# Kernel optimization log

Hardware: AMD Instinct MI355X
Metric: run time of the kernel (lower is better)

## Reference

```python
import jax, jax.numpy as jnp
import numpy as np

# Sampled-block sizes (fanouts [25, 10], batch of 1024 seeds)
N_SRC1, N_DST1, N_E1 = 292864, 11264, 281600
N_DST2, N_E2 = 1024, 10240
IN, H, C = 256, 256, 47


def setup_inputs() -> dict:
    key = jax.random.key(0)
    ks = jax.random.split(key, 9)
    s_in = 1.0 / np.sqrt(IN)
    s_h = 1.0 / np.sqrt(H)
    x = jax.random.normal(ks[0], (N_SRC1, IN), jnp.float32)
    src1 = jax.random.randint(ks[1], (N_E1,), 0, N_SRC1)
    dst1 = jnp.sort(jax.random.randint(ks[2], (N_E1,), 0, N_DST1))
    src2 = jax.random.randint(ks[3], (N_E2,), 0, N_DST1)
    dst2 = jnp.sort(jax.random.randint(ks[4], (N_E2,), 0, N_DST2))
    return dict(
        x=x, src1=src1, dst1=dst1, src2=src2, dst2=dst2,
        W_self1=jax.random.normal(ks[5], (IN, H), jnp.float32) * s_in,
        W_neigh1=jax.random.normal(ks[6], (IN, H), jnp.float32) * s_in,
        b1=jnp.zeros((H,), jnp.float32),
        W_self2=jax.random.normal(ks[7], (H, C), jnp.float32) * s_h,
        W_neigh2=jax.random.normal(ks[8], (H, C), jnp.float32) * s_h,
        b2=jnp.zeros((C,), jnp.float32),
    )


def _sage_mean(h_src, src, dst, n_dst, W_self, W_neigh, b):
    # DGL SAGEConv(mean): out = fc_self(h_dst) + fc_neigh(mean_{neighbors} h_src) + b
    gathered = h_src[src]                                   # [E, F] gather
    agg = jax.ops.segment_sum(gathered, dst, num_segments=n_dst)
    deg = jax.ops.segment_sum(jnp.ones((src.shape[0],), h_src.dtype), dst,
                              num_segments=n_dst)
    h_neigh = agg / jnp.maximum(deg, 1.0)[:, None]          # mean aggregation
    h_dst = h_src[:n_dst]                                   # dst nodes are prefix of src
    return h_dst @ W_self + h_neigh @ W_neigh + b


def reference(x, src1, dst1, src2, dst2,
              W_self1, W_neigh1, b1, W_self2, W_neigh2, b2):
    h = _sage_mean(x, src1, dst1, N_DST1, W_self1, W_neigh1, b1)
    h = jax.nn.relu(h)  # dropout is identity in eval mode
    out = _sage_mean(h, src2, dst2, N_DST2, W_self2, W_neigh2, b2)
    return out
```

## Files before the change

### kernel.cpp

```cpp
#include <hip/hip_runtime.h>

#define NSRC1 292864
#define NDST1 11264
#define NE1   281600
#define NDST2 1024
#define NE2   10240

typedef __bf16 bf16x8 __attribute__((ext_vector_type(8)));
typedef float  f32x4  __attribute__((ext_vector_type(4)));

__device__ __forceinline__ unsigned short f2bf(float f) {
    union { float f; unsigned u; } v; v.f = f;
    unsigned r = v.u + 0x7FFF + ((v.u >> 16) & 1);
    return (unsigned short)(r >> 16);
}

__device__ __forceinline__ void acc4(float4& a, const float4& v) {
    a.x += v.x; a.y += v.y; a.z += v.z; a.w += v.w;
}

__global__ __launch_bounds__(256) void prep_kernel(
    const int* __restrict__ dst1, const int* __restrict__ dst2,
    const float* __restrict__ Ws, const float* __restrict__ Wn,
    int* __restrict__ rp1, int* __restrict__ rp2,
    unsigned short* __restrict__ Wt)
{
    __shared__ float t[64][65];
    if (blockIdx.x < 1140) {
        const int tid = blockIdx.x * 256 + threadIdx.x;
        if (tid < NE1) {
            const int d  = dst1[tid];
            const int dp = (tid == 0) ? -1 : dst1[tid - 1];
            for (int j = dp + 1; j <= d; ++j) rp1[j] = tid;
            if (tid == NE1 - 1) for (int j = d + 1; j <= NDST1; ++j) rp1[j] = NE1;
        } else {
            const int e  = tid - NE1;
            const int d  = dst2[e];
            const int dp = (e == 0) ? -1 : dst2[e - 1];
            for (int j = dp + 1; j <= d; ++j) rp2[j] = e;
            if (e == NE2 - 1) for (int j = d + 1; j <= NDST2; ++j) rp2[j] = NE2;
        }
        return;
    }
    const int tileid = blockIdx.x - 1140;
    const int kb = (tileid & 7) * 64, nb = (tileid >> 3) * 64;
    const float* __restrict__ W = (kb < 256) ? Ws : Wn;
    const int kofs = (kb < 256) ? kb : kb - 256;
    const int c  = threadIdx.x & 63;
    const int r0 = threadIdx.x >> 6;
    #pragma unroll
    for (int i = 0; i < 16; ++i) {
        const int r = r0 + i * 4;
        t[r][c] = W[(size_t)(kofs + r) * 256 + nb + c];
    }
    __syncthreads();
    #pragma unroll
    for (int i = 0; i < 16; ++i) {
        const int r = r0 + i * 4;
        Wt[(size_t)(nb + r) * 512 + kb + c] = f2bf(t[c][r]);
    }
}

__global__ __launch_bounds__(256) void agg1_fused_kernel(
    const float* __restrict__ x,
    const int*   __restrict__ src_idx,
    const int*   __restrict__ rowptr,
    unsigned short* __restrict__ Abf)
{
    const int lane = threadIdx.x & 63;
    const int w    = threadIdx.x >> 6;
    const int d    = blockIdx.x * 4 + w;

    const int start = rowptr[d];
    const int end   = rowptr[d + 1];

    const float4* __restrict__ xcol = (const float4*)x + lane;

    const float4 xv = xcol[(size_t)d * 64];

    float4 a0 = make_float4(0.f,0.f,0.f,0.f);
    float4 a1 = a0, a2 = a0, a3 = a0, a4 = a0, a5 = a0, a6 = a0, a7 = a0;

    for (int base = start; base < end; base += 64) {
        const int nb = (end - base < 64) ? (end - base) : 64;
        int my = (lane < nb) ? src_idx[base + lane] : 0;
        int j = 0;
        for (; j + 8 <= nb; j += 8) {
            const int s0 = __builtin_amdgcn_readlane(my, j + 0);
            const int s1 = __builtin_amdgcn_readlane(my, j + 1);
            const int s2 = __builtin_amdgcn_readlane(my, j + 2);
            const int s3 = __builtin_amdgcn_readlane(my, j + 3);
            const int s4 = __builtin_amdgcn_readlane(my, j + 4);
            const int s5 = __builtin_amdgcn_readlane(my, j + 5);
            const int s6 = __builtin_amdgcn_readlane(my, j + 6);
            const int s7 = __builtin_amdgcn_readlane(my, j + 7);
            const float4 v0 = xcol[(size_t)s0 * 64];
            const float4 v1 = xcol[(size_t)s1 * 64];
            const float4 v2 = xcol[(size_t)s2 * 64];
            const float4 v3 = xcol[(size_t)s3 * 64];
            const float4 v4 = xcol[(size_t)s4 * 64];
            const float4 v5 = xcol[(size_t)s5 * 64];
            const float4 v6 = xcol[(size_t)s6 * 64];
            const float4 v7 = xcol[(size_t)s7 * 64];
            acc4(a0, v0); acc4(a1, v1); acc4(a2, v2); acc4(a3, v3);
            acc4(a4, v4); acc4(a5, v5); acc4(a6, v6); acc4(a7, v7);
        }
        if (j + 4 <= nb) {
            const int s0 = __builtin_amdgcn_readlane(my, j + 0);
            const int s1 = __builtin_amdgcn_readlane(my, j + 1);
            const int s2 = __builtin_amdgcn_readlane(my, j + 2);
            const int s3 = __builtin_amdgcn_readlane(my, j + 3);
            const float4 v0 = xcol[(size_t)s0 * 64];
            const float4 v1 = xcol[(size_t)s1 * 64];
            const float4 v2 = xcol[(size_t)s2 * 64];
            const float4 v3 = xcol[(size_t)s3 * 64];
            acc4(a0, v0); acc4(a1, v1); acc4(a2, v2); acc4(a3, v3);
            j += 4;
        }
        for (; j < nb; ++j) {
            const int s = __builtin_amdgcn_readlane(my, j);
            acc4(a0, xcol[(size_t)s * 64]);
        }
    }
    acc4(a0, a1); acc4(a2, a3); acc4(a4, a5); acc4(a6, a7);
    acc4(a0, a2); acc4(a4, a6); acc4(a0, a4);

    const int deg = end - start;
    const float inv = 1.0f / (deg > 0 ? (float)deg : 1.0f);

    ushort4 nbv;
    nbv.x = f2bf(a0.x * inv); nbv.y = f2bf(a0.y * inv);
    nbv.z = f2bf(a0.z * inv); nbv.w = f2bf(a0.w * inv);
    *(ushort4*)(Abf + (size_t)d * 512 + 256 + lane * 4) = nbv;

    ushort4 sf;
    sf.x = f2bf(xv.x); sf.y = f2bf(xv.y); sf.z = f2bf(xv.z); sf.w = f2bf(xv.w);
    *(ushort4*)(Abf + (size_t)d * 512 + lane * 4) = sf;
}

#define LDT 40

__global__ __launch_bounds__(256) void gemm1_mfma_kernel(
    const unsigned short* __restrict__ Abf,
    const unsigned short* __restrict__ Wt,
    const float* __restrict__ bias,
    float* __restrict__ h)
{
    __shared__ unsigned short As[64][LDT];
    __shared__ unsigned short Bs[64][LDT];

    const int tid  = threadIdx.x;
    const int lane = tid & 63;
    const int w    = tid >> 6;
    const int wm   = (w & 1) * 32;
    const int wn   = (w >> 1) * 32;
    const int mblk = blockIdx.x * 64;
    const int nblk = blockIdx.y * 64;

    const int r16 = lane & 15;
    const int k0  = (lane >> 4) * 8;

    f32x4 acc[2][2] = {};

    for (int kt = 0; kt < 512; kt += 32) {
        {
            const int r  = tid >> 2;
            const int kk = (tid & 3) * 8;
            *(uint4*)&As[r][kk] =
                *(const uint4*)(Abf + (size_t)(mblk + r) * 512 + kt + kk);
            *(uint4*)&Bs[r][kk] =
                *(const uint4*)(Wt + (size_t)(nblk + r) * 512 + kt + kk);
        }
        __syncthreads();

        bf16x8 bfrag[2];
        #pragma unroll
        for (int ni = 0; ni < 2; ++ni)
            bfrag[ni] = *(const bf16x8*)&Bs[wn + ni * 16 + r16][k0];
        #pragma unroll
        for (int mi = 0; mi < 2; ++mi) {
            const bf16x8 afrag = *(const bf16x8*)&As[wm + mi * 16 + r16][k0];
            #pragma unroll
            for (int ni = 0; ni < 2; ++ni)
                acc[mi][ni] = __builtin_amdgcn_mfma_f32_16x16x32_bf16(
                    afrag, bfrag[ni], acc[mi][ni], 0, 0, 0);
        }
        __syncthreads();
    }

    #pragma unroll
    for (int mi = 0; mi < 2; ++mi) {
        #pragma unroll
        for (int ni = 0; ni < 2; ++ni) {
            const int col = nblk + wn + ni * 16 + r16;
            const float bb = bias[col];
            #pragma unroll
            for (int r = 0; r < 4; ++r) {
                const int row = mblk + wm + mi * 16 + (lane >> 4) * 4 + r;
                const float v = acc[mi][ni][r] + bb;
                h[(size_t)row * 256 + col] = v > 0.f ? v : 0.f;
            }
        }
    }
}

__global__ __launch_bounds__(256) void layer2_kernel(
    const float* __restrict__ h,
    const int*   __restrict__ src_idx,
    const int*   __restrict__ rowptr,
    const float* __restrict__ Ws,
    const float* __restrict__ Wn,
    const float* __restrict__ b,
    float* __restrict__ out)
{
    __shared__ float hn[4][260];
    __shared__ float hs[4][260];

    const int lane = threadIdx.x & 63;
    const int w    = threadIdx.x >> 6;
    const int m    = blockIdx.x * 4 + w;

    const int start = rowptr[m];
    const int end   = rowptr[m + 1];

    const float4* __restrict__ hcol = (const float4*)h + lane;

    const float4 sv = hcol[(size_t)m * 64];

    float4 a0 = make_float4(0.f,0.f,0.f,0.f);
    float4 a1 = a0, a2 = a0, a3 = a0;

    for (int base = start; base < end; base += 64) {
        const int nb = (end - base < 64) ? (end - base) : 64;
        int my = (lane < nb) ? src_idx[base + lane] : 0;
        int j = 0;
        for (; j + 4 <= nb; j += 4) {
            const int s0 = __builtin_amdgcn_readlane(my, j + 0);
            const int s1 = __builtin_amdgcn_readlane(my, j + 1);
            const int s2 = __builtin_amdgcn_readlane(my, j + 2);
            const int s3 = __builtin_amdgcn_readlane(my, j + 3);
            const float4 v0 = hcol[(size_t)s0 * 64];
            const float4 v1 = hcol[(size_t)s1 * 64];
            const float4 v2 = hcol[(size_t)s2 * 64];
            const float4 v3 = hcol[(size_t)s3 * 64];
            acc4(a0, v0); acc4(a1, v1); acc4(a2, v2); acc4(a3, v3);
        }
        for (; j < nb; ++j) {
            const int s = __builtin_amdgcn_readlane(my, j);
            acc4(a0, hcol[(size_t)s * 64]);
        }
    }
    acc4(a0, a1); acc4(a2, a3); acc4(a0, a2);

    const int deg = end - start;
    const float inv = 1.0f / (deg > 0 ? (float)deg : 1.0f);
    a0.x *= inv; a0.y *= inv; a0.z *= inv; a0.w *= inv;
    *(float4*)&hn[w][lane * 4] = a0;
    *(float4*)&hs[w][lane * 4] = sv;
    __syncthreads();

    if (lane < 47) {
        float acc = b[lane];
        #pragma unroll 4
        for (int k = 0; k < 256; ++k) {
            acc += hs[w][k] * Ws[k * 47 + lane] + hn[w][k] * Wn[k * 47 + lane];
        }
        out[(size_t)m * 47 + lane] = acc;
    }
}

extern "C" void kernel_launch(void* const* d_in, const int* in_sizes, int n_in,
                              void* d_out, int out_size, void* d_ws, size_t ws_size,
                              hipStream_t stream) {
    const float* x    = (const float*)d_in[0];
    const int*   src1 = (const int*)  d_in[1];
    const int*   dst1 = (const int*)  d_in[2];
    const int*   src2 = (const int*)  d_in[3];
    const int*   dst2 = (const int*)  d_in[4];
    const float* Ws1  = (const float*)d_in[5];
    const float* Wn1  = (const float*)d_in[6];
    const float* b1   = (const float*)d_in[7];
    const float* Ws2  = (const float*)d_in[8];
    const float* Wn2  = (const float*)d_in[9];
    const float* b2   = (const float*)d_in[10];
    float* out = (float*)d_out;

    char* ws = (char*)d_ws;
    const size_t sz_Abf = (size_t)NDST1 * 512 * sizeof(unsigned short);
    const size_t sz_h   = (size_t)NDST1 * 256 * sizeof(float);
    const size_t sz_Wt  = (size_t)256 * 512 * sizeof(unsigned short);
    const size_t sz_rp1 = (size_t)(NDST1 + 2) * sizeof(int);
    unsigned short* Abf = (unsigned short*)(ws);
    float*          h   = (float*)(ws + sz_Abf);
    unsigned short* Wt  = (unsigned short*)(ws + sz_Abf + sz_h);
    int*            rp1 = (int*)(ws + sz_Abf + sz_h + sz_Wt);
    int*            rp2 = (int*)(ws + sz_Abf + sz_h + sz_Wt + sz_rp1);

    prep_kernel<<<1172, 256, 0, stream>>>(dst1, dst2, Ws1, Wn1, rp1, rp2, Wt);
    agg1_fused_kernel<<<NDST1 / 4, 256, 0, stream>>>(x, src1, rp1, Abf);
    dim3 g1(NDST1 / 64, 256 / 64);
    gemm1_mfma_kernel<<<g1, 256, 0, stream>>>(Abf, Wt, b1, h);
    layer2_kernel<<<NDST2 / 4, 256, 0, stream>>>(h, src2, rp2, Ws2, Wn2, b2, out);
}
```

Baseline: 440.3 us.

## Fuse layer-1 neighbor aggregation into the MFMA GEMM via shared-memory A tile

Merges the gather/mean aggregation kernel and the layer-1 GEMM into one kernel. Each block aggregates 16 destination rows into an LDS A tile in bf16, then multiplies it by all 256 output columns using MFMA. This removes the global Abf round trip and one kernel launch. In exchange each block streams the full weight matrix from global/L2 per 16 rows, and the block count drops, which can reduce parallelism for the latency-bound gather.

New measurement: 441.2 us (median of 2 runs). No clear change (+0.2%).

```diff
diff --git a/kernel.cpp b/kernel.cpp
--- a/kernel.cpp
+++ b/kernel.cpp
@@ -61,145 +61,128 @@
     }
 }
 
-__global__ __launch_bounds__(256) void agg1_fused_kernel(
+__global__ __launch_bounds__(256) void agg_gemm1_kernel(
     const float* __restrict__ x,
     const int*   __restrict__ src_idx,
     const int*   __restrict__ rowptr,
-    unsigned short* __restrict__ Abf)
-{
-    const int lane = threadIdx.x & 63;
-    const int w    = threadIdx.x >> 6;
-    const int d    = blockIdx.x * 4 + w;
-
-    const int start = rowptr[d];
-    const int end   = rowptr[d + 1];
-
-    const float4* __restrict__ xcol = (const float4*)x + lane;
-
-    const float4 xv = xcol[(size_t)d * 64];
-
-    float4 a0 = make_float4(0.f,0.f,0.f,0.f);
-    float4 a1 = a0, a2 = a0, a3 = a0, a4 = a0, a5 = a0, a6 = a0, a7 = a0;
-
-    for (int base = start; base < end; base += 64) {
-        const int nb = (end - base < 64) ? (end - base) : 64;
-        int my = (lane < nb) ? src_idx[base + lane] : 0;
-        int j = 0;
-        for (; j + 8 <= nb; j += 8) {
-            const int s0 = __builtin_amdgcn_readlane(my, j + 0);
-            const int s1 = __builtin_amdgcn_readlane(my, j + 1);
-            const int s2 = __builtin_amdgcn_readlane(my, j + 2);
-            const int s3 = __builtin_amdgcn_readlane(my, j + 3);
-            const int s4 = __builtin_amdgcn_readlane(my, j + 4);
-            const int s5 = __builtin_amdgcn_readlane(my, j + 5);
-            const int s6 = __builtin_amdgcn_readlane(my, j + 6);
-            const int s7 = __builtin_amdgcn_readlane(my, j + 7);
-            const float4 v0 = xcol[(size_t)s0 * 64];
-            const float4 v1 = xcol[(size_t)s1 * 64];
-            const float4 v2 = xcol[(size_t)s2 * 64];
-            const float4 v3 = xcol[(size_t)s3 * 64];
-            const float4 v4 = xcol[(size_t)s4 * 64];
-            const float4 v5 = xcol[(size_t)s5 * 64];
-            const float4 v6 = xcol[(size_t)s6 * 64];
-            const float4 v7 = xcol[(size_t)s7 * 64];
-            acc4(a0, v0); acc4(a1, v1); acc4(a2, v2); acc4(a3, v3);
-            acc4(a4, v4); acc4(a5, v5); acc4(a6, v6); acc4(a7, v7);
-        }
-        if (j + 4 <= nb) {
-            const int s0 = __builtin_amdgcn_readlane(my, j + 0);
-            const int s1 = __builtin_amdgcn_readlane(my, j + 1);
-            const int s2 = __builtin_amdgcn_readlane(my, j + 2);
-            const int s3 = __builtin_amdgcn_readlane(my, j + 3);
-            const float4 v0 = xcol[(size_t)s0 * 64];
-            const float4 v1 = xcol[(size_t)s1 * 64];
-            const float4 v2 = xcol[(size_t)s2 * 64];
-            const float4 v3 = xcol[(size_t)s3 * 64];
-            acc4(a0, v0); acc4(a1, v1); acc4(a2, v2); acc4(a3, v3);
-            j += 4;
-        }
-        for (; j < nb; ++j) {
-            const int s = __builtin_amdgcn_readlane(my, j);
-            acc4(a0, xcol[(size_t)s * 64]);
-        }
-    }
-    acc4(a0, a1); acc4(a2, a3); acc4(a4, a5); acc4(a6, a7);
-    acc4(a0, a2); acc4(a4, a6); acc4(a0, a4);
-
-    const int deg = end - start;
-    const float inv = 1.0f / (deg > 0 ? (float)deg : 1.0f);
-
-    ushort4 nbv;
-    nbv.x = f2bf(a0.x * inv); nbv.y = f2bf(a0.y * inv);
-    nbv.z = f2bf(a0.z * inv); nbv.w = f2bf(a0.w * inv);
-    *(ushort4*)(Abf + (size_t)d * 512 + 256 + lane * 4) = nbv;
-
-    ushort4 sf;
-    sf.x = f2bf(xv.x); sf.y = f2bf(xv.y); sf.z = f2bf(xv.z); sf.w = f2bf(xv.w);
-    *(ushort4*)(Abf + (size_t)d * 512 + lane * 4) = sf;
-}
-
-#define LDT 40
-
-__global__ __launch_bounds__(256) void gemm1_mfma_kernel(
-    const unsigned short* __restrict__ Abf,
     const unsigned short* __restrict__ Wt,
     const float* __restrict__ bias,
     float* __restrict__ h)
 {
-    __shared__ unsigned short As[64][LDT];
-    __shared__ unsigned short Bs[64][LDT];
+    __shared__ unsigned short As[16][520];
+    __shared__ unsigned short Bs[256][40];
 
     const int tid  = threadIdx.x;
     const int lane = tid & 63;
     const int w    = tid >> 6;
-    const int wm   = (w & 1) * 32;
-    const int wn   = (w >> 1) * 32;
-    const int mblk = blockIdx.x * 64;
-    const int nblk = blockIdx.y * 64;
+    const int mblk = blockIdx.x * 16;
+
+    const float4* __restrict__ xcol = (const float4*)x + lane;
+
+    for (int i = 0; i < 4; ++i) {
+        const int lr = w * 4 + i;
+        const int d  = mblk + lr;
+
+        const int start = rowptr[d];
+        const int end   = rowptr[d + 1];
+
+        const float4 xv = xcol[(size_t)d * 64];
+
+        float4 a0 = make_float4(0.f,0.f,0.f,0.f);
+        float4 a1 = a0, a2 = a0, a3 = a0, a4 = a0, a5 = a0, a6 = a0, a7 = a0;
+
+        for (int base = start; base < end; base += 64) {
+            const int nb = (end - base < 64) ? (end - base) : 64;
+            int my = (lane < nb) ? src_idx[base + lane] : 0;
+            int j = 0;
+            for (; j + 8 <= nb; j += 8) {
+                const int s0 = __builtin_amdgcn_readlane(my, j + 0);
+                const int s1 = __builtin_amdgcn_readlane(my, j + 1);
+                const int s2 = __builtin_amdgcn_readlane(my, j + 2);
+                const int s3 = __builtin_amdgcn_readlane(my, j + 3);
+                const int s4 = __builtin_amdgcn_readlane(my, j + 4);
+                const int s5 = __builtin_amdgcn_readlane(my, j + 5);
+                const int s6 = __builtin_amdgcn_readlane(my, j + 6);
+                const int s7 = __builtin_amdgcn_readlane(my, j + 7);
+                const float4 v0 = xcol[(size_t)s0 * 64];
+                const float4 v1 = xcol[(size_t)s1 * 64];
+                const float4 v2 = xcol[(size_t)s2 * 64];
+                const float4 v3 = xcol[(size_t)s3 * 64];
+                const float4 v4 = xcol[(size_t)s4 * 64];
+                const float4 v5 = xcol[(size_t)s5 * 64];
+                const float4 v6 = xcol[(size_t)s6 * 64];
+                const float4 v7 = xcol[(size_t)s7 * 64];
+                acc4(a0, v0); acc4(a1, v1); acc4(a2, v2); acc4(a3, v3);
+                acc4(a4, v4); acc4(a5, v5); acc4(a6, v6); acc4(a7, v7);
+            }
+            if (j + 4 <= nb) {
+                const int s0 = __builtin_amdgcn_readlane(my, j + 0);
+                const int s1 = __builtin_amdgcn_readlane(my, j + 1);
+                const int s2 = __builtin_amdgcn_readlane(my, j + 2);
+                const int s3 = __builtin_amdgcn_readlane(my, j + 3);
+                const float4 v0 = xcol[(size_t)s0 * 64];
+                const float4 v1 = xcol[(size_t)s1 * 64];
+                const float4 v2 = xcol[(size_t)s2 * 64];
+                const float4 v3 = xcol[(size_t)s3 * 64];
+                acc4(a0, v0); acc4(a1, v1); acc4(a2, v2); acc4(a3, v3);
+                j += 4;
+            }
+            for (; j < nb; ++j) {
+                const int s = __builtin_amdgcn_readlane(my, j);
+                acc4(a0, xcol[(size_t)s * 64]);
+            }
+        }
+        acc4(a0, a1); acc4(a2, a3); acc4(a4, a5); acc4(a6, a7);
+        acc4(a0, a2); acc4(a4, a6); acc4(a0, a4);
+
+        const int deg = end - start;
+        const float inv = 1.0f / (deg > 0 ? (float)deg : 1.0f);
+
+        ushort4 sf;
+        sf.x = f2bf(xv.x); sf.y = f2bf(xv.y); sf.z = f2bf(xv.z); sf.w = f2bf(xv.w);
+        *(ushort4*)&As[lr][lane * 4] = sf;
+
+        ushort4 nbv;
+        nbv.x = f2bf(a0.x * inv); nbv.y = f2bf(a0.y * inv);
+        nbv.z = f2bf(a0.z * inv); nbv.w = f2bf(a0.w * inv);
+        *(ushort4*)&As[lr][256 + lane * 4] = nbv;
+    }
 
     const int r16 = lane & 15;
     const int k0  = (lane >> 4) * 8;
 
-    f32x4 acc[2][2] = {};
+    f32x4 acc[4] = {};
 
     for (int kt = 0; kt < 512; kt += 32) {
-        {
-            const int r  = tid >> 2;
-            const int kk = (tid & 3) * 8;
-            *(uint4*)&As[r][kk] =
-                *(const uint4*)(Abf + (size_t)(mblk + r) * 512 + kt + kk);
-            *(uint4*)&Bs[r][kk] =
-                *(const uint4*)(Wt + (size_t)(nblk + r) * 512 + kt + kk);
+        #pragma unroll
+        for (int i = 0; i < 4; ++i) {
+            const int idx  = tid + i * 256;
+            const int row  = idx >> 2;
+            const int koff = (idx & 3) * 8;
+            *(uint4*)&Bs[row][koff] =
+                *(const uint4*)(Wt + (size_t)row * 512 + kt + koff);
         }
         __syncthreads();
 
-        bf16x8 bfrag[2];
+        const bf16x8 afrag = *(const bf16x8*)&As[r16][kt + k0];
         #pragma unroll
-        for (int ni = 0; ni < 2; ++ni)
-            bfrag[ni] = *(const bf16x8*)&Bs[wn + ni * 16 + r16][k0];
+        for (int ni = 0; ni < 4; ++ni) {
+            const bf16x8 bfrag = *(const bf16x8*)&Bs[w * 64 + ni * 16 + r16][k0];
+            acc[ni] = __builtin_amdgcn_mfma_f32_16x16x32_bf16(
+                afrag, bfrag, acc[ni], 0, 0, 0);
+        }
+        __syncthreads();
+    }
+
+    #pragma unroll
+    for (int ni = 0; ni < 4; ++ni) {
+        const int col = w * 64 + ni * 16 + r16;
+        const float bb = bias[col];
         #pragma unroll
-        for (int mi = 0; mi < 2; ++mi) {
-            const bf16x8 afrag = *(const bf16x8*)&As[wm + mi * 16 + r16][k0];
-            #pragma unroll
-            for (int ni = 0; ni < 2; ++ni)
-                acc[mi][ni] = __builtin_amdgcn_mfma_f32_16x16x32_bf16(
-                    afrag, bfrag[ni], acc[mi][ni], 0, 0, 0);
-        }
-        __syncthreads();
-    }
-
-    #pragma unroll
-    for (int mi = 0; mi < 2; ++mi) {
-        #pragma unroll
-        for (int ni = 0; ni < 2; ++ni) {
-            const int col = nblk + wn + ni * 16 + r16;
-            const float bb = bias[col];
-            #pragma unroll
-            for (int r = 0; r < 4; ++r) {
-                const int row = mblk + wm + mi * 16 + (lane >> 4) * 4 + r;
-                const float v = acc[mi][ni][r] + bb;
-                h[(size_t)row * 256 + col] = v > 0.f ? v : 0.f;
-            }
+        for (int r = 0; r < 4; ++r) {
+            const int row = mblk + (lane >> 4) * 4 + r;
+            const float v = acc[ni][r] + bb;
+            h[(size_t)row * 256 + col] = v > 0.f ? v : 0.f;
         }
     }
 }
@@ -286,19 +269,15 @@
     float* out = (float*)d_out;
 
     char* ws = (char*)d_ws;
-    const size_t sz_Abf = (size_t)NDST1 * 512 * sizeof(unsigned short);
     const size_t sz_h   = (size_t)NDST1 * 256 * sizeof(float);
     const size_t sz_Wt  = (size_t)256 * 512 * sizeof(unsigned short);
     const size_t sz_rp1 = (size_t)(NDST1 + 2) * sizeof(int);
-    unsigned short* Abf = (unsigned short*)(ws);
-    float*          h   = (float*)(ws + sz_Abf);
-    unsigned short* Wt  = (unsigned short*)(ws + sz_Abf + sz_h);
-    int*            rp1 = (int*)(ws + sz_Abf + sz_h + sz_Wt);
-    int*            rp2 = (int*)(ws + sz_Abf + sz_h + sz_Wt + sz_rp1);
+    float*          h   = (float*)(ws);
+    unsigned short* Wt  = (unsigned short*)(ws + sz_h);
+    int*            rp1 = (int*)(ws + sz_h + sz_Wt);
+    int*            rp2 = (int*)(ws + sz_h + sz_Wt + sz_rp1);
 
     prep_kernel<<<1172, 256, 0, stream>>>(dst1, dst2, Ws1, Wn1, rp1, rp2, Wt);
-    agg1_fused_kernel<<<NDST1 / 4, 256, 0, stream>>>(x, src1, rp1, Abf);
-    dim3 g1(NDST1 / 64, 256 / 64);
-    gemm1_mfma_kernel<<<g1, 256, 0, stream>>>(Abf, Wt, b1, h);
+    agg_gemm1_kernel<<<NDST1 / 16, 256, 0, stream>>>(x, src1, rp1, Wt, b1, h);
     layer2_kernel<<<NDST2 / 4, 256, 0, stream>>>(h, src2, rp2, Ws2, Wn2, b2, out);
 }
```
